# Kernel tuning notes

Measured on AMD Instinct MI355X. Metric: run time of the kernel, lower is better.

Reference implementation:

```python
import jax, jax.numpy as jnp
import numpy as np

EPS = 1e-12


def setup_inputs() -> dict:
    key = jax.random.key(0)
    k1, k2 = jax.random.split(key)
    N, K, D = 32768, 2048, 512
    node_repr = jax.random.normal(k1, (N, D), dtype=jnp.float32)
    mask = jnp.ones((N, 1), dtype=jnp.float32)
    # nn.Embedding weight for the centroids (euclidean branch: exp_map_zero is identity)
    centroid_weight = jax.random.normal(k2, (K, D), dtype=jnp.float32)
    return {"node_repr": node_repr, "mask": mask, "centroid_weight": centroid_weight}


def reference(node_repr, mask, centroid_weight):
    # Euclidean manifold: exp_map_zero(x) = x; distance(x, y) = ||x - y||_2.
    # The torch code expands to [N*K, D]; here we fuse via the Gram-matrix identity
    x2 = jnp.sum(node_repr * node_repr, axis=-1, keepdims=True)        # [N, 1]
    c2 = jnp.sum(centroid_weight * centroid_weight, axis=-1)           # [K]
    xc = jnp.einsum('nd,kd->nk', node_repr, centroid_weight)           # [N, K] GEMM
    d2 = x2 + c2[None, :] - 2.0 * xc                                   # [N, K]
    dist = jnp.sqrt(jnp.maximum(d2, EPS))                              # [N, K]
    node_centroid_dist = dist[None, :, :] * mask[None, :, :]           # [1, N, K] (mask broadcasts [1,N,1])
    graph_centroid_dist = jnp.sum(node_centroid_dist, axis=1) / jnp.sum(mask)  # [1, K]
    return graph_centroid_dist, node_centroid_dist
```

## Files before the change

kernel.cpp:

```cpp
#include <hip/hip_runtime.h>
#include <hip/hip_bf16.h>
#include <math.h>

typedef __bf16 bf16_t;
typedef __bf16 bf16x4 __attribute__((ext_vector_type(4)));
typedef __bf16 bf16x8 __attribute__((ext_vector_type(8)));
typedef float floatx4 __attribute__((ext_vector_type(4)));

#define N_NODES 32768
#define K_CENT  2048
#define D_DIM   512

__global__ void prep_rows_kernel(const float* __restrict__ src,
                                 bf16_t* __restrict__ dst,
                                 float* __restrict__ sq) {
  const int w = threadIdx.x >> 6;
  const int l = threadIdx.x & 63;
  const int row = blockIdx.x * 4 + w;
  const float4* s = (const float4*)(src + (size_t)row * D_DIM);
  float4 f0 = s[l];
  float4 f1 = s[64 + l];
  bf16x4 b0 = { (bf16_t)f0.x, (bf16_t)f0.y, (bf16_t)f0.z, (bf16_t)f0.w };
  bf16x4 b1 = { (bf16_t)f1.x, (bf16_t)f1.y, (bf16_t)f1.z, (bf16_t)f1.w };
  bf16x4* d = (bf16x4*)(dst + (size_t)row * D_DIM);
  d[l] = b0;
  d[64 + l] = b1;
  float v = f0.x*f0.x + f0.y*f0.y + f0.z*f0.z + f0.w*f0.w
          + f1.x*f1.x + f1.y*f1.y + f1.z*f1.z + f1.w*f1.w;
  #pragma unroll
  for (int s2 = 32; s2; s2 >>= 1) v += __shfl_xor(v, s2);
  if (l == 0) sq[row] = v;
}

__global__ void mask_sum_kernel(const float* __restrict__ m,
                                float* __restrict__ out, int n) {
  float v = 0.f;
  for (int i = blockIdx.x * blockDim.x + threadIdx.x; i < n;
       i += gridDim.x * blockDim.x)
    v += m[i];
  #pragma unroll
  for (int s = 32; s; s >>= 1) v += __shfl_xor(v, s);
  __shared__ float red[4];
  if ((threadIdx.x & 63) == 0) red[threadIdx.x >> 6] = v;
  __syncthreads();
  if (threadIdx.x == 0) atomicAdd(out, red[0] + red[1] + red[2] + red[3]);
}

__device__ inline void gld_lds16(const void* g, void* l) {
  __builtin_amdgcn_global_load_lds(
      (__attribute__((address_space(1))) void*)const_cast<void*>(g),
      (__attribute__((address_space(3))) void*)l, 16, 0, 0);
}

__global__ void __launch_bounds__(256)
gemm_dist_kernel(const bf16_t* __restrict__ A,
                 const bf16_t* __restrict__ B,
                 const float* __restrict__ x2,
                 const float* __restrict__ c2,
                 const float* __restrict__ mask,
                 float* __restrict__ out_node,
                 float* __restrict__ colsum) {
  __shared__ __align__(16) bf16_t sA[128 * 64];
  __shared__ __align__(16) bf16_t sB[128 * 64];

  const int t = threadIdx.x;
  const int w = t >> 6;
  const int l = t & 63;
  const int bm = blockIdx.y;
  const int bn = blockIdx.x;
  const int wm = (w >> 1) * 64;
  const int wn = (w & 1) * 64;
  const int lr = l & 15;
  const int lk = (l >> 4) * 8;

  floatx4 acc[4][4] = {};

  const int srow = w * 8 + (l >> 3);
  const int scol = (l & 7) * 8;
  const bf16_t* gA = A + (size_t)(bm * 128 + srow) * D_DIM + scol;
  const bf16_t* gB = B + (size_t)(bn * 128 + srow) * D_DIM + scol;
  char* lA = (char*)sA + w * 1024;
  char* lB = (char*)sB + w * 1024;

  for (int kt = 0; kt < D_DIM; kt += 64) {
    #pragma unroll
    for (int p = 0; p < 4; ++p) {
      gld_lds16(gA + (size_t)(p * 32) * D_DIM + kt, lA + p * 4096);
      gld_lds16(gB + (size_t)(p * 32) * D_DIM + kt, lB + p * 4096);
    }
    __syncthreads();
    #pragma unroll
    for (int ks = 0; ks < 64; ks += 32) {
      bf16x8 af[4], bfr[4];
      #pragma unroll
      for (int i = 0; i < 4; ++i)
        af[i] = *(const bf16x8*)&sA[(wm + i * 16 + lr) * 64 + ks + lk];
      #pragma unroll
      for (int j = 0; j < 4; ++j)
        bfr[j] = *(const bf16x8*)&sB[(wn + j * 16 + lr) * 64 + ks + lk];
      #pragma unroll
      for (int i = 0; i < 4; ++i) {
        #pragma unroll
        for (int j = 0; j < 4; ++j)
          acc[i][j] = __builtin_amdgcn_mfma_f32_16x16x32_bf16(
              af[i], bfr[j], acc[i][j], 0, 0, 0);
      }
    }
    __syncthreads();
  }

  const int col0 = bn * 128 + wn;
  float c2v[4];
  #pragma unroll
  for (int j = 0; j < 4; ++j) c2v[j] = c2[col0 + j * 16 + lr];

  float colacc[4] = {0.f, 0.f, 0.f, 0.f};
  #pragma unroll
  for (int i = 0; i < 4; ++i) {
    const int rbase = bm * 128 + wm + i * 16 + (l >> 4) * 4;
    #pragma unroll
    for (int r = 0; r < 4; ++r) {
      const int row = rbase + r;
      const float xv = x2[row];
      const float mk = mask[row];
      float* orow = out_node + (size_t)row * K_CENT + col0 + lr;
      #pragma unroll
      for (int j = 0; j < 4; ++j) {
        float d2 = xv + c2v[j] - 2.0f * acc[i][j][r];
        float dist = sqrtf(fmaxf(d2, 1e-12f));
        float dm = dist * mk;
        orow[j * 16] = dm;
        colacc[j] += dm;
      }
    }
  }

  #pragma unroll
  for (int j = 0; j < 4; ++j) {
    colacc[j] += __shfl_xor(colacc[j], 16);
    colacc[j] += __shfl_xor(colacc[j], 32);
  }
  float* colbuf = (float*)sA;
  if (w < 2 && l < 16) {
    #pragma unroll
    for (int j = 0; j < 4; ++j) colbuf[wn + j * 16 + l] = colacc[j];
  }
  __syncthreads();
  if (w >= 2 && l < 16) {
    #pragma unroll
    for (int j = 0; j < 4; ++j) colbuf[wn + j * 16 + l] += colacc[j];
  }
  __syncthreads();
  if (t < 128) atomicAdd(&colsum[bn * 128 + t], colbuf[t]);
}

__global__ void finalize_kernel(const float* __restrict__ colsum,
                                const float* __restrict__ msum,
                                float* __restrict__ out) {
  int k = blockIdx.x * 256 + threadIdx.x;
  out[k] = colsum[k] / msum[0];
}

extern "C" void kernel_launch(void* const* d_in, const int* in_sizes, int n_in,
                              void* d_out, int out_size, void* d_ws, size_t ws_size,
                              hipStream_t stream) {
  const float* node = (const float*)d_in[0];
  const float* mask = (const float*)d_in[1];
  const float* cent = (const float*)d_in[2];
  float* out_graph = (float*)d_out;
  float* out_node  = out_graph + K_CENT;

  char* ws = (char*)d_ws;
  size_t off = 0;
  bf16_t* Abf = (bf16_t*)(ws + off); off += (size_t)N_NODES * D_DIM * sizeof(bf16_t);
  bf16_t* Cbf = (bf16_t*)(ws + off); off += (size_t)K_CENT * D_DIM * sizeof(bf16_t);
  float* x2     = (float*)(ws + off); off += (size_t)N_NODES * sizeof(float);
  float* c2     = (float*)(ws + off); off += (size_t)K_CENT * sizeof(float);
  float* colsum = (float*)(ws + off); off += (size_t)K_CENT * sizeof(float);
  float* msum   = (float*)(ws + off); off += sizeof(float);

  hipMemsetAsync(colsum, 0, (K_CENT + 1) * sizeof(float), stream);

  prep_rows_kernel<<<N_NODES / 4, 256, 0, stream>>>(node, Abf, x2);
  prep_rows_kernel<<<K_CENT / 4, 256, 0, stream>>>(cent, Cbf, c2);
  mask_sum_kernel<<<64, 256, 0, stream>>>(mask, msum, N_NODES);
  gemm_dist_kernel<<<dim3(16, 256), 256, 0, stream>>>(
      Abf, Cbf, x2, c2, mask, out_node, colsum);
  finalize_kernel<<<K_CENT / 256, 256, 0, stream>>>(colsum, msum, out_graph);
}
```

Measured before the change: 422.0 us.

## Rewrite GEMM mainloop with 256x256 tiles, 4-stage LDS pipeline and swizzle

Enlarges the block tile to 256x256 with 8 waves, each wave owning a 128x64 sub-tile. Operand loads now go through a 4-deep ring buffer of 32-wide K slices, overlapping global-to-LDS copies with MFMA work by using explicit vmcnt waits in place of full syncthreads. It also XOR-swizzles the LDS layout to avoid bank conflicts, remaps block IDs for L2 locality, and raises MFMA priority with setprio. In exchange it uses more registers (128 accumulator floats per lane) and 128 KB of LDS, which lowers occupancy, and the hand-counted waits are fragile if the load counts change.

```diff
diff --git a/kernel.cpp b/kernel.cpp
--- a/kernel.cpp
+++ b/kernel.cpp
@@ -52,7 +52,11 @@
       (__attribute__((address_space(3))) void*)l, 16, 0, 0);
 }
 
-__global__ void __launch_bounds__(256)
+#define S_WAITV8 asm volatile("s_waitcnt vmcnt(8)" ::: "memory")
+#define S_WAITV4 asm volatile("s_waitcnt vmcnt(4)" ::: "memory")
+#define S_WAITV0 asm volatile("s_waitcnt vmcnt(0)" ::: "memory")
+
+__global__ void __launch_bounds__(512, 2)
 gemm_dist_kernel(const bf16_t* __restrict__ A,
                  const bf16_t* __restrict__ B,
                  const float* __restrict__ x2,
@@ -60,64 +64,107 @@
                  const float* __restrict__ mask,
                  float* __restrict__ out_node,
                  float* __restrict__ colsum) {
-  __shared__ __align__(16) bf16_t sA[128 * 64];
-  __shared__ __align__(16) bf16_t sB[128 * 64];
+  __shared__ __align__(16) bf16_t sA[4][256 * 32];
+  __shared__ __align__(16) bf16_t sB[4][256 * 32];
 
   const int t = threadIdx.x;
   const int w = t >> 6;
   const int l = t & 63;
-  const int bm = blockIdx.y;
-  const int bn = blockIdx.x;
-  const int wm = (w >> 1) * 64;
-  const int wn = (w & 1) * 64;
   const int lr = l & 15;
-  const int lk = (l >> 4) * 8;
-
-  floatx4 acc[4][4] = {};
-
-  const int srow = w * 8 + (l >> 3);
-  const int scol = (l & 7) * 8;
-  const bf16_t* gA = A + (size_t)(bm * 128 + srow) * D_DIM + scol;
-  const bf16_t* gB = B + (size_t)(bn * 128 + srow) * D_DIM + scol;
-  char* lA = (char*)sA + w * 1024;
-  char* lB = (char*)sB + w * 1024;
-
-  for (int kt = 0; kt < D_DIM; kt += 64) {
-    #pragma unroll
-    for (int p = 0; p < 4; ++p) {
-      gld_lds16(gA + (size_t)(p * 32) * D_DIM + kt, lA + p * 4096);
-      gld_lds16(gB + (size_t)(p * 32) * D_DIM + kt, lB + p * 4096);
-    }
-    __syncthreads();
-    #pragma unroll
-    for (int ks = 0; ks < 64; ks += 32) {
-      bf16x8 af[4], bfr[4];
-      #pragma unroll
-      for (int i = 0; i < 4; ++i)
-        af[i] = *(const bf16x8*)&sA[(wm + i * 16 + lr) * 64 + ks + lk];
+  const int hi = l >> 4;
+
+  const int wg = (blockIdx.x & 7) * 128 + (blockIdx.x >> 3);
+  const int bm = wg >> 3;
+  const int bn = wg & 7;
+
+  const int wm = (w >> 2) * 128;
+  const int wn = (w & 3) * 64;
+
+  floatx4 acc[8][4] = {};
+
+  const int srow = t >> 2;
+  const int scolE = (((t & 3) ^ ((t >> 3) & 3)) << 3);
+  const bf16_t* gA = A + (size_t)(bm * 256 + srow) * D_DIM + scolE;
+  const bf16_t* gB = B + (size_t)(bn * 256 + srow) * D_DIM + scolE;
+  char* ldsAw = (char*)sA + w * 1024;
+  char* ldsBw = (char*)sB + w * 1024;
+
+  auto stageA = [&](int kt) {
+    const int sb = (kt & 3) * 16384;
+    #pragma unroll
+    for (int q = 0; q < 2; ++q)
+      gld_lds16(gA + (size_t)(q * 128) * D_DIM + kt * 32,
+                ldsAw + sb + q * 8192);
+  };
+  auto stageB = [&](int kt) {
+    const int sb = (kt & 3) * 16384;
+    #pragma unroll
+    for (int q = 0; q < 2; ++q)
+      gld_lds16(gB + (size_t)(q * 128) * D_DIM + kt * 32,
+                ldsBw + sb + q * 8192);
+  };
+
+  const int cOff = ((hi ^ ((lr >> 1) & 3)) << 4);
+  const int aRow = wm + lr;
+  const int bRow = wn + lr;
+
+  auto tile = [&](int kt, bool doStage) {
+    const char* aS = (const char*)sA + (kt & 3) * 16384;
+    const char* bS = (const char*)sB + (kt & 3) * 16384;
+    bf16x8 af[4], bfr[4];
+    if (doStage) stageA(kt + 3);
+    #pragma unroll
+    for (int j = 0; j < 4; ++j)
+      bfr[j] = *(const bf16x8*)(bS + ((bRow + j * 16) << 6) + cOff);
+    #pragma unroll
+    for (int i = 0; i < 4; ++i)
+      af[i] = *(const bf16x8*)(aS + ((aRow + i * 16) << 6) + cOff);
+    __builtin_amdgcn_s_setprio(1);
+    #pragma unroll
+    for (int i = 0; i < 4; ++i)
       #pragma unroll
       for (int j = 0; j < 4; ++j)
-        bfr[j] = *(const bf16x8*)&sB[(wn + j * 16 + lr) * 64 + ks + lk];
+        acc[i][j] = __builtin_amdgcn_mfma_f32_16x16x32_bf16(
+            af[i], bfr[j], acc[i][j], 0, 0, 0);
+    __builtin_amdgcn_s_setprio(0);
+    __builtin_amdgcn_s_barrier();
+    if (doStage) stageB(kt + 3);
+    #pragma unroll
+    for (int i = 0; i < 4; ++i)
+      af[i] = *(const bf16x8*)(aS + ((aRow + 64 + i * 16) << 6) + cOff);
+    __builtin_amdgcn_s_setprio(1);
+    #pragma unroll
+    for (int i = 0; i < 4; ++i)
       #pragma unroll
-      for (int i = 0; i < 4; ++i) {
-        #pragma unroll
-        for (int j = 0; j < 4; ++j)
-          acc[i][j] = __builtin_amdgcn_mfma_f32_16x16x32_bf16(
-              af[i], bfr[j], acc[i][j], 0, 0, 0);
-      }
-    }
-    __syncthreads();
-  }
-
-  const int col0 = bn * 128 + wn;
+      for (int j = 0; j < 4; ++j)
+        acc[4 + i][j] = __builtin_amdgcn_mfma_f32_16x16x32_bf16(
+            af[i], bfr[j], acc[4 + i][j], 0, 0, 0);
+    __builtin_amdgcn_s_setprio(0);
+  };
+
+  stageA(0); stageB(0); stageA(1); stageB(1); stageA(2); stageB(2);
+  S_WAITV8;
+  __builtin_amdgcn_s_barrier();
+
+  #pragma unroll 1
+  for (int kt = 0; kt < 13; ++kt) {
+    tile(kt, true);
+    S_WAITV8;
+    __builtin_amdgcn_s_barrier();
+  }
+  tile(13, false); S_WAITV4; __builtin_amdgcn_s_barrier();
+  tile(14, false); S_WAITV0; __builtin_amdgcn_s_barrier();
+  tile(15, false);
+
+  const int col0 = bn * 256 + wn;
   float c2v[4];
   #pragma unroll
   for (int j = 0; j < 4; ++j) c2v[j] = c2[col0 + j * 16 + lr];
 
   float colacc[4] = {0.f, 0.f, 0.f, 0.f};
   #pragma unroll
-  for (int i = 0; i < 4; ++i) {
-    const int rbase = bm * 128 + wm + i * 16 + (l >> 4) * 4;
+  for (int ai = 0; ai < 8; ++ai) {
+    const int rbase = bm * 256 + wm + ai * 16 + hi * 4;
     #pragma unroll
     for (int r = 0; r < 4; ++r) {
       const int row = rbase + r;
@@ -126,7 +173,7 @@
       float* orow = out_node + (size_t)row * K_CENT + col0 + lr;
       #pragma unroll
       for (int j = 0; j < 4; ++j) {
-        float d2 = xv + c2v[j] - 2.0f * acc[i][j][r];
+        float d2 = xv + c2v[j] - 2.0f * acc[ai][j][r];
         float dist = sqrtf(fmaxf(d2, 1e-12f));
         float dm = dist * mk;
         orow[j * 16] = dm;
@@ -140,18 +187,19 @@
     colacc[j] += __shfl_xor(colacc[j], 16);
     colacc[j] += __shfl_xor(colacc[j], 32);
   }
+  __syncthreads();
   float* colbuf = (float*)sA;
-  if (w < 2 && l < 16) {
+  if ((w >> 2) == 0 && l < 16) {
     #pragma unroll
     for (int j = 0; j < 4; ++j) colbuf[wn + j * 16 + l] = colacc[j];
   }
   __syncthreads();
-  if (w >= 2 && l < 16) {
+  if ((w >> 2) == 1 && l < 16) {
     #pragma unroll
     for (int j = 0; j < 4; ++j) colbuf[wn + j * 16 + l] += colacc[j];
   }
   __syncthreads();
-  if (t < 128) atomicAdd(&colsum[bn * 128 + t], colbuf[t]);
+  if (t < 256) atomicAdd(&colsum[bn * 256 + t], colbuf[t]);
 }
 
 __global__ void finalize_kernel(const float* __restrict__ colsum,
@@ -184,7 +232,7 @@
   prep_rows_kernel<<<N_NODES / 4, 256, 0, stream>>>(node, Abf, x2);
   prep_rows_kernel<<<K_CENT / 4, 256, 0, stream>>>(cent, Cbf, c2);
   mask_sum_kernel<<<64, 256, 0, stream>>>(mask, msum, N_NODES);
-  gemm_dist_kernel<<<dim3(16, 256), 256, 0, stream>>>(
+  gemm_dist_kernel<<<1024, 512, 0, stream>>>(
       Abf, Cbf, x2, c2, mask, out_node, colsum);
   finalize_kernel<<<K_CENT / 256, 256, 0, stream>>>(colsum, msum, out_graph);
 }
```

Result: faster. 413.1 us (-2.1%).
